# Optimization experiments

Measured on AMD Instinct MI355X. Metric: run time of the kernel, lower is better.

The kernel has to match this reference:

```python
import jax, jax.numpy as jnp
import numpy as np

WS = 16        # window size
NH = 8         # num heads
EPS = 1e-6
BN_EPS = 1e-5


def _l2norm(t):
    # normalize along the channel (d) axis, which is axis=-2, per position
    return t / jnp.linalg.norm(t, axis=-2, keepdims=True)


def setup_inputs() -> dict:
    key = jax.random.key(0)
    k1, k2, k3 = jax.random.split(key, 3)
    B, C, H, W = 8, 96, 256, 256
    x = jax.random.normal(k1, (B, C, H, W), dtype=jnp.float32)
    w_qkv = jax.random.normal(k2, (3 * C, C), dtype=jnp.float32) * (1.0 / np.sqrt(C))
    w_proj = jax.random.normal(k3, (C, C), dtype=jnp.float32) * (1.0 / np.sqrt(C))
    gamma = jnp.ones((C,), dtype=jnp.float32)
    beta = jnp.zeros((C,), dtype=jnp.float32)
    return {"x": x, "w_qkv": w_qkv, "w_proj": w_proj, "gamma": gamma, "beta": beta}


def reference(x, w_qkv, w_proj, gamma, beta):
    B, C, H, W = x.shape
    ws, nh = WS, NH
    d = C // nh
    # pad H, W up to multiples of ws (static shapes -> jit-safe)
    Hp = (H + ws - 1) // ws * ws
    Wp = (W + ws - 1) // ws * ws
    if (Hp, Wp) != (H, W):
        x = jnp.pad(x, ((0, 0), (0, 0), (0, Hp - H), (0, Wp - W)))
    hh, ww = Hp // ws, Wp // ws

    # 1x1 conv qkv projection (no bias)
    qkv = jnp.einsum('oc,bchw->bohw', w_qkv, x)  # [B, 3C, Hp, Wp]
    # rearrange 'b (qkv h d) (hh ws1) (ww ws2) -> qkv (b hh ww) h d (ws1 ws2)'
    qkv = qkv.reshape(B, 3, nh, d, hh, ws, ww, ws)
    qkv = qkv.transpose(1, 0, 4, 6, 2, 3, 5, 7).reshape(3, B * hh * ww, nh, d, ws * ws)
    q, k, v = qkv[0], qkv[1], qkv[2]  # each [bw, h, d, n]  (n = ws*ws)

    q = _l2norm(q).transpose(0, 1, 3, 2)  # [bw, h, n, d]
    k = _l2norm(k)                        # [bw, h, d, n]

    ksum = k.sum(axis=-1) + EPS           # [bw, h, d]
    tailor = 1.0 / (ws * ws + jnp.einsum('bhnc,bhc->bhn', q, ksum))  # [bw, h, n]

    kv = jnp.einsum('bhmn,bhcn->bhmc', k, v)     # [bw, h, d, d]
    attn = jnp.einsum('bhnm,bhmc->bhcn', q, kv)  # [bw, h, d, n]
    attn = attn + v.sum(axis=-1, keepdims=True)  # broadcast sum_n v over n
    attn = attn * tailor[:, :, None, :]

    # rearrange '(b hh ww) h d (ws1 ws2) -> b (h d) (hh ws1) (ww ws2)'
    out = attn.reshape(B, hh, ww, nh, d, ws, ws)
    out = out.transpose(0, 3, 4, 1, 5, 2, 6).reshape(B, C, Hp, Wp)
    out = out[:, :, :H, :W]

    # proj: 1x1 conv + BatchNorm2d (training-mode batch statistics)
    y = jnp.einsum('oc,bchw->bohw', w_proj, out)
    mean = y.mean(axis=(0, 2, 3), keepdims=True)
    var = y.var(axis=(0, 2, 3), keepdims=True)
    y = (y - mean) * jax.lax.rsqrt(var + BN_EPS)
    y = y * gamma[None, :, None, None] + beta[None, :, None, None]
    return y
```

## Files before the change

kernel.cpp:

```cpp
#include <hip/hip_runtime.h>

typedef short s8v __attribute__((ext_vector_type(8)));
typedef float f4v __attribute__((ext_vector_type(4)));

union F8 { int4 i; s8v s; };
union F8L { long long l[2]; s8v s; };

__device__ __forceinline__ short f2bf(float f){
  union {float f; unsigned u;} v; v.f = f;
  unsigned r = (v.u + 0x7FFFu + ((v.u >> 16) & 1u)) >> 16;
  return (short)r;
}

#define MFMA(a,b,c) __builtin_amdgcn_mfma_f32_16x16x32_bf16((a),(b),(c),0,0,0)

#define WS_W2_OFF   58368
#define WS_ST_OFF   82944
#define WS_OUT_OFF  (1u<<20)

__global__ void prep_kernel(const float* __restrict__ wqkv, const float* __restrict__ wproj,
                            unsigned short* __restrict__ w1, unsigned short* __restrict__ w2p,
                            float* __restrict__ stats){
  int i = blockIdx.x * 256 + threadIdx.x;
  for (int j = i; j < 304*96; j += gridDim.x * 256){
    int row = j / 96, c = j - row * 96;
    float v = (row < 288) ? wqkv[row * 96 + c] : 0.f;
    w1[j] = (unsigned short)f2bf(v);
  }
  for (int j = i; j < 96*128; j += gridDim.x * 256){
    int o = j >> 7, c = j & 127, h = c >> 4, ii = c & 15;
    float v = (ii < 12) ? wproj[o * 96 + h * 12 + ii] : 0.f;
    w2p[j] = (unsigned short)f2bf(v);
  }
  if (i < 192) stats[i] = 0.f;
}

__global__ __launch_bounds__(256,4) void attn_kernel(const float* __restrict__ x,
                                                     const unsigned short* __restrict__ w1,
                                                     short* __restrict__ outp){
  __shared__ short ks[2][16*264];
  __shared__ short vs[2][16*264];

  const int tid  = threadIdx.x;
  const int lane = tid & 63, wave = tid >> 6;
  const int quad = lane >> 4, col = lane & 15;
  const int wx = blockIdx.x, wy = blockIdx.y, b = blockIdx.z;
  const int h0 = wy * 16, w0 = wx * 16;

  for (int i = tid; i < 2*4*264; i += 256){
    int buf = i / (4*264), j = i % (4*264);
    int r = 12 + j / 264, cc = j % 264;
    short v = (r == 15) ? (short)0x3F80 : (short)0;
    ks[buf][r*264 + cc] = v; vs[buf][r*264 + cc] = v;
  }

  const float* xb = x + ((size_t)b * 96 << 16);
  s8v Bf[4][3];
  #pragma unroll
  for (int jt = 0; jt < 4; ++jt){
    int t0 = wave * 64 + jt * 16;
    const float* px = xb + (size_t)(h0 + (t0 >> 4)) * 256 + (w0 + col);
    #pragma unroll
    for (int kt = 0; kt < 3; ++kt){
      F8 f;
      #pragma unroll
      for (int j = 0; j < 8; ++j){
        int c = kt * 32 + quad * 8 + j;
        f.s[j] = f2bf(px[(size_t)c << 16]);
      }
      Bf[jt][kt] = f.s;
    }
  }

  for (int h = 0; h < 8; ++h){
    const int p = h & 1;
    s8v bq[4];
    {
      s8v Aq[3];
      #pragma unroll
      for (int kt = 0; kt < 3; ++kt){
        F8 f; f.i = *(const int4*)(w1 + (h*12 + col) * 96 + kt*32 + quad*8);
        Aq[kt] = f.s;
      }
      #pragma unroll
      for (int jt = 0; jt < 4; ++jt){
        f4v a = {0.f,0.f,0.f,0.f};
        #pragma unroll
        for (int kt = 0; kt < 3; ++kt) a = MFMA(Aq[kt], Bf[jt][kt], a);
        float s = (quad < 3) ? (a[0]*a[0] + a[1]*a[1] + a[2]*a[2] + a[3]*a[3]) : 0.f;
        s += __shfl_xor(s, 16, 64); s += __shfl_xor(s, 32, 64);
        float rq = rsqrtf(s);
        float q0 = a[0]*rq, q1 = a[1]*rq, q2 = a[2]*rq, q3 = a[3]*rq;
        int s0 = (quad == 0) ? col        : (32 + col);
        int s1 = (quad == 0) ? (16 + col) : (32 + col);
        float v0 = __shfl(q0, s0, 64), v1 = __shfl(q1, s0, 64);
        float v2 = __shfl(q2, s0, 64), v3 = __shfl(q3, s0, 64);
        float w4 = __shfl(q0, s1, 64), w5 = __shfl(q1, s1, 64);
        float w6 = __shfl(q2, s1, 64), w7 = __shfl(q3, s1, 64);
        F8 f;
        bool lo = (quad < 2);
        f.s[0] = lo ? f2bf(v0) : (short)0;
        f.s[1] = lo ? f2bf(v1) : (short)0;
        f.s[2] = lo ? f2bf(v2) : (short)0;
        f.s[3] = lo ? f2bf(v3) : (short)0;
        f.s[4] = (quad == 0) ? f2bf(w4) : ((quad == 1) ? (short)0x3F80 : (short)0);
        f.s[5] = (quad == 0) ? f2bf(w5) : (short)0;
        f.s[6] = (quad == 0) ? f2bf(w6) : (short)0;
        f.s[7] = (quad == 0) ? f2bf(w7) : (short)0;
        bq[jt] = f.s;
      }
    }
    {
      s8v Ak[3];
      #pragma unroll
      for (int kt = 0; kt < 3; ++kt){
        F8 f; f.i = *(const int4*)(w1 + (96 + h*12 + col) * 96 + kt*32 + quad*8);
        Ak[kt] = f.s;
      }
      #pragma unroll
      for (int jt = 0; jt < 4; ++jt){
        f4v a = {0.f,0.f,0.f,0.f};
        #pragma unroll
        for (int kt = 0; kt < 3; ++kt) a = MFMA(Ak[kt], Bf[jt][kt], a);
        float s = (quad < 3) ? (a[0]*a[0] + a[1]*a[1] + a[2]*a[2] + a[3]*a[3]) : 0.f;
        s += __shfl_xor(s, 16, 64); s += __shfl_xor(s, 32, 64);
        float rk = rsqrtf(s);
        if (quad < 3){
          int t = wave*64 + jt*16 + col;
          #pragma unroll
          for (int r = 0; r < 4; ++r) ks[p][(quad*4 + r)*264 + t] = f2bf(a[r]*rk);
        }
      }
    }
    {
      s8v Av[3];
      #pragma unroll
      for (int kt = 0; kt < 3; ++kt){
        F8 f; f.i = *(const int4*)(w1 + (192 + h*12 + col) * 96 + kt*32 + quad*8);
        Av[kt] = f.s;
      }
      #pragma unroll
      for (int jt = 0; jt < 4; ++jt){
        f4v a = {0.f,0.f,0.f,0.f};
        #pragma unroll
        for (int kt = 0; kt < 3; ++kt) a = MFMA(Av[kt], Bf[jt][kt], a);
        if (quad < 3){
          int t = wave*64 + jt*16 + col;
          #pragma unroll
          for (int r = 0; r < 4; ++r) vs[p][(quad*4 + r)*264 + t] = f2bf(a[r]);
        }
      }
    }
    __syncthreads();

    f4v kvv = {0.f,0.f,0.f,0.f};
    #pragma unroll
    for (int kk = 0; kk < 8; ++kk){
      F8 a, bv;
      a.i  = *(const int4*)&ks[p][col*264 + kk*32 + quad*8];
      bv.i = *(const int4*)&vs[p][col*264 + kk*32 + quad*8];
      kvv = MFMA(a.s, bv.s, kvv);
    }
    F8 fa;
    {
      int cc = (col == 12) ? 15 : col;
      int l0 = ((quad << 1) << 4) | cc;
      int l1 = (((quad << 1) + 1) << 4) | cc;
      float v;
      v = __shfl(kvv[0], l0 & 63, 64); fa.s[0] = f2bf((quad < 2) ? v : 0.f);
      v = __shfl(kvv[1], l0 & 63, 64); fa.s[1] = f2bf((quad < 2) ? v : 0.f);
      v = __shfl(kvv[2], l0 & 63, 64); fa.s[2] = f2bf((quad < 2) ? v : 0.f);
      v = __shfl(kvv[3], l0 & 63, 64); fa.s[3] = f2bf((quad < 2) ? v : 0.f);
      float v0  = __shfl(kvv[0], l1 & 63, 64);
      float v15 = __shfl(kvv[3], 48 | cc, 64);
      fa.s[4] = f2bf((quad == 0) ? v0 : ((quad == 1) ? v15 : 0.f));
      v = __shfl(kvv[1], l1 & 63, 64); fa.s[5] = f2bf((quad == 0) ? v : 0.f);
      v = __shfl(kvv[2], l1 & 63, 64); fa.s[6] = f2bf((quad == 0) ? v : 0.f);
      v = __shfl(kvv[3], l1 & 63, 64); fa.s[7] = f2bf((quad == 0) ? v : 0.f);
    }
    #pragma unroll
    for (int jt = 0; jt < 4; ++jt){
      int t0 = wave*64 + jt*16;
      f4v z = {0.f,0.f,0.f,0.f};
      f4v d2 = MFMA(fa.s, bq[jt], z);
      float dot = __shfl(d2[0], 48 + col, 64);
      float tl = 1.f / dot;
      if (quad < 3){
        int pix = (h0 + (t0 >> 4)) * 256 + (w0 + col);
        short* po = outp + ((size_t)((b*8 + h) * 65536 + pix)) * 12 + quad*4;
        short4 pk; pk.x = f2bf(d2[0]*tl); pk.y = f2bf(d2[1]*tl); pk.z = f2bf(d2[2]*tl); pk.w = f2bf(d2[3]*tl);
        *(short4*)po = pk;
      }
    }
  }
}

__device__ __forceinline__ void load_proj_bfrag(const short* __restrict__ outp,
                                                int b, int pixrow, int wave, int quad, int col,
                                                s8v Bf[4][4]){
  #pragma unroll
  for (int jt = 0; jt < 4; ++jt){
    int pix = pixrow + wave*64 + jt*16 + col;
    #pragma unroll
    for (int kt = 0; kt < 4; ++kt){
      int h = kt*2 + (quad >> 1);
      const short* pb = outp + ((size_t)((b*8 + h) * 65536 + pix)) * 12;
      F8L f;
      if ((quad & 1) == 0){ f.l[0] = *(const long long*)(pb);     f.l[1] = *(const long long*)(pb + 4); }
      else                { f.l[0] = *(const long long*)(pb + 8); f.l[1] = 0; }
      Bf[jt][kt] = f.s;
    }
  }
}

__global__ __launch_bounds__(256,4) void projstats_kernel(const short* __restrict__ outp,
                                                          const unsigned short* __restrict__ w2p,
                                                          float* __restrict__ stats){
  __shared__ float sld[192];
  const int tid = threadIdx.x;
  if (tid < 192) sld[tid] = 0.f;
  __syncthreads();
  const int lane = tid & 63, wave = tid >> 6;
  const int quad = lane >> 4, col = lane & 15;
  const int hrow = blockIdx.x, b = blockIdx.y;

  s8v Bf[4][4];
  load_proj_bfrag(outp, b, hrow*256, wave, quad, col, Bf);

  #pragma unroll
  for (int mt = 0; mt < 6; ++mt){
    s8v Af[4];
    #pragma unroll
    for (int kt = 0; kt < 4; ++kt){
      F8 f; f.i = *(const int4*)(w2p + (mt*16 + col)*128 + kt*32 + quad*8);
      Af[kt] = f.s;
    }
    float rs[4] = {0.f,0.f,0.f,0.f}, rss[4] = {0.f,0.f,0.f,0.f};
    #pragma unroll
    for (int jt = 0; jt < 4; ++jt){
      f4v a = {0.f,0.f,0.f,0.f};
      #pragma unroll
      for (int kt = 0; kt < 4; ++kt) a = MFMA(Af[kt], Bf[jt][kt], a);
      #pragma unroll
      for (int r = 0; r < 4; ++r){ float v = a[r]; rs[r] += v; rss[r] += v*v; }
    }
    #pragma unroll
    for (int r = 0; r < 4; ++r){
      float a1 = rs[r], a2 = rss[r];
      a1 += __shfl_xor(a1, 1, 64); a2 += __shfl_xor(a2, 1, 64);
      a1 += __shfl_xor(a1, 2, 64); a2 += __shfl_xor(a2, 2, 64);
      a1 += __shfl_xor(a1, 4, 64); a2 += __shfl_xor(a2, 4, 64);
      a1 += __shfl_xor(a1, 8, 64); a2 += __shfl_xor(a2, 8, 64);
      if (col == 0){
        int o = mt*16 + quad*4 + r;
        atomicAdd(&sld[o], a1);
        atomicAdd(&sld[96 + o], a2);
      }
    }
  }
  __syncthreads();
  if (tid < 192) atomicAdd(&stats[tid], sld[tid]);
}

__global__ __launch_bounds__(256,4) void projbn_kernel(const short* __restrict__ outp,
                                                       const unsigned short* __restrict__ w2p,
                                                       const float* __restrict__ stats,
                                                       const float* __restrict__ gamma,
                                                       const float* __restrict__ beta,
                                                       float* __restrict__ y){
  __shared__ float sc[96], sh[96];
  const int tid = threadIdx.x;
  if (tid < 96){
    const float invN = 1.f / 524288.f;
    float m  = stats[tid] * invN;
    float var = stats[96 + tid] * invN - m*m;
    float s = gamma[tid] * rsqrtf(var + 1e-5f);
    sc[tid] = s; sh[tid] = beta[tid] - m * s;
  }
  __syncthreads();
  const int lane = tid & 63, wave = tid >> 6;
  const int quad = lane >> 4, col = lane & 15;
  const int hrow = blockIdx.x, b = blockIdx.y;

  s8v Bf[4][4];
  load_proj_bfrag(outp, b, hrow*256, wave, quad, col, Bf);

  float* yb = y + ((size_t)(b*96) << 16) + (size_t)hrow * 256;
  #pragma unroll
  for (int mt = 0; mt < 6; ++mt){
    s8v Af[4];
    #pragma unroll
    for (int kt = 0; kt < 4; ++kt){
      F8 f; f.i = *(const int4*)(w2p + (mt*16 + col)*128 + kt*32 + quad*8);
      Af[kt] = f.s;
    }
    #pragma unroll
    for (int jt = 0; jt < 4; ++jt){
      int n0 = wave*64 + jt*16;
      f4v a = {0.f,0.f,0.f,0.f};
      #pragma unroll
      for (int kt = 0; kt < 4; ++kt) a = MFMA(Af[kt], Bf[jt][kt], a);
      #pragma unroll
      for (int r = 0; r < 4; ++r){
        int ch = mt*16 + quad*4 + r;
        yb[((size_t)ch << 16) + n0 + col] = a[r] * sc[ch] + sh[ch];
      }
    }
  }
}

extern "C" void kernel_launch(void* const* d_in, const int* in_sizes, int n_in,
                              void* d_out, int out_size, void* d_ws, size_t ws_size,
                              hipStream_t stream){
  const float* x     = (const float*)d_in[0];
  const float* wqkv  = (const float*)d_in[1];
  const float* wproj = (const float*)d_in[2];
  const float* gamma = (const float*)d_in[3];
  const float* beta  = (const float*)d_in[4];
  char* ws = (char*)d_ws;
  unsigned short* w1  = (unsigned short*)(ws);
  unsigned short* w2p = (unsigned short*)(ws + WS_W2_OFF);
  float* stats = (float*)(ws + WS_ST_OFF);
  short* outp  = (short*)(ws + WS_OUT_OFF);
  float* y = (float*)d_out;

  hipLaunchKernelGGL(prep_kernel, dim3(64), dim3(256), 0, stream, wqkv, wproj, w1, w2p, stats);
  hipLaunchKernelGGL(attn_kernel, dim3(16, 16, 8), dim3(256), 0, stream, x, w1, outp);
  hipLaunchKernelGGL(projstats_kernel, dim3(256, 8), dim3(256), 0, stream, outp, w2p, stats);
  hipLaunchKernelGGL(projbn_kernel, dim3(256, 8), dim3(256), 0, stream, outp, w2p, stats, gamma, beta, y);
}
```

Baseline: 543.3 us.

## Single-buffer attention LDS, halve proj tiles per block, and slice BN stat atomics

The attention kernel drops its K/V LDS double buffer in favour of one buffer plus an extra barrier per head, and its launch bounds are raised to 8 blocks per CU to allow higher occupancy. The projection kernels now give each block half a row of pixels (32 per wave), doubling the grid and halving register fragments, with launch bounds raised to 6. BatchNorm statistics are spread over 16 slices to reduce global atomic contention, and the BN kernel sums the slices. In exchange the attention kernel pays an extra barrier per head and loses overlap between heads.

```diff
diff --git a/kernel.cpp b/kernel.cpp
--- a/kernel.cpp
+++ b/kernel.cpp
@@ -16,6 +16,7 @@
 
 #define WS_W2_OFF   58368
 #define WS_ST_OFF   82944
+#define N_STAT_SLICES 16
 #define WS_OUT_OFF  (1u<<20)
 
 __global__ void prep_kernel(const float* __restrict__ wqkv, const float* __restrict__ wproj,
@@ -32,14 +33,14 @@
     float v = (ii < 12) ? wproj[o * 96 + h * 12 + ii] : 0.f;
     w2p[j] = (unsigned short)f2bf(v);
   }
-  if (i < 192) stats[i] = 0.f;
-}
-
-__global__ __launch_bounds__(256,4) void attn_kernel(const float* __restrict__ x,
+  if (i < 192 * N_STAT_SLICES) stats[i] = 0.f;
+}
+
+__global__ __launch_bounds__(256,8) void attn_kernel(const float* __restrict__ x,
                                                      const unsigned short* __restrict__ w1,
                                                      short* __restrict__ outp){
-  __shared__ short ks[2][16*264];
-  __shared__ short vs[2][16*264];
+  __shared__ short ks[16*264];
+  __shared__ short vs[16*264];
 
   const int tid  = threadIdx.x;
   const int lane = tid & 63, wave = tid >> 6;
@@ -47,11 +48,10 @@
   const int wx = blockIdx.x, wy = blockIdx.y, b = blockIdx.z;
   const int h0 = wy * 16, w0 = wx * 16;
 
-  for (int i = tid; i < 2*4*264; i += 256){
-    int buf = i / (4*264), j = i % (4*264);
-    int r = 12 + j / 264, cc = j % 264;
+  for (int i = tid; i < 4*264; i += 256){
+    int r = 12 + i / 264, cc = i % 264;
     short v = (r == 15) ? (short)0x3F80 : (short)0;
-    ks[buf][r*264 + cc] = v; vs[buf][r*264 + cc] = v;
+    ks[r*264 + cc] = v; vs[r*264 + cc] = v;
   }
 
   const float* xb = x + ((size_t)b * 96 << 16);
@@ -73,7 +73,6 @@
   }
 
   for (int h = 0; h < 8; ++h){
-    const int p = h & 1;
     s8v bq[4];
     {
       s8v Aq[3];
@@ -110,6 +109,7 @@
         bq[jt] = f.s;
       }
     }
+    __syncthreads();
     {
       s8v Ak[3];
       #pragma unroll
@@ -128,7 +128,7 @@
         if (quad < 3){
           int t = wave*64 + jt*16 + col;
           #pragma unroll
-          for (int r = 0; r < 4; ++r) ks[p][(quad*4 + r)*264 + t] = f2bf(a[r]*rk);
+          for (int r = 0; r < 4; ++r) ks[(quad*4 + r)*264 + t] = f2bf(a[r]*rk);
         }
       }
     }
@@ -147,7 +147,7 @@
         if (quad < 3){
           int t = wave*64 + jt*16 + col;
           #pragma unroll
-          for (int r = 0; r < 4; ++r) vs[p][(quad*4 + r)*264 + t] = f2bf(a[r]);
+          for (int r = 0; r < 4; ++r) vs[(quad*4 + r)*264 + t] = f2bf(a[r]);
         }
       }
     }
@@ -157,8 +157,8 @@
     #pragma unroll
     for (int kk = 0; kk < 8; ++kk){
       F8 a, bv;
-      a.i  = *(const int4*)&ks[p][col*264 + kk*32 + quad*8];
-      bv.i = *(const int4*)&vs[p][col*264 + kk*32 + quad*8];
+      a.i  = *(const int4*)&ks[col*264 + kk*32 + quad*8];
+      bv.i = *(const int4*)&vs[col*264 + kk*32 + quad*8];
       kvv = MFMA(a.s, bv.s, kvv);
     }
     F8 fa;
@@ -196,11 +196,11 @@
 }
 
 __device__ __forceinline__ void load_proj_bfrag(const short* __restrict__ outp,
-                                                int b, int pixrow, int wave, int quad, int col,
-                                                s8v Bf[4][4]){
+                                                int b, int pix0, int quad, int col,
+                                                s8v Bf[2][4]){
   #pragma unroll
-  for (int jt = 0; jt < 4; ++jt){
-    int pix = pixrow + wave*64 + jt*16 + col;
+  for (int jt = 0; jt < 2; ++jt){
+    int pix = pix0 + jt*16 + col;
     #pragma unroll
     for (int kt = 0; kt < 4; ++kt){
       int h = kt*2 + (quad >> 1);
@@ -213,7 +213,7 @@
   }
 }
 
-__global__ __launch_bounds__(256,4) void projstats_kernel(const short* __restrict__ outp,
+__global__ __launch_bounds__(256,6) void projstats_kernel(const short* __restrict__ outp,
                                                           const unsigned short* __restrict__ w2p,
                                                           float* __restrict__ stats){
   __shared__ float sld[192];
@@ -224,8 +224,8 @@
   const int quad = lane >> 4, col = lane & 15;
   const int hrow = blockIdx.x, b = blockIdx.y;
 
-  s8v Bf[4][4];
-  load_proj_bfrag(outp, b, hrow*256, wave, quad, col, Bf);
+  s8v Bf[2][4];
+  load_proj_bfrag(outp, b, hrow*128 + wave*32, quad, col, Bf);
 
   #pragma unroll
   for (int mt = 0; mt < 6; ++mt){
@@ -237,7 +237,7 @@
     }
     float rs[4] = {0.f,0.f,0.f,0.f}, rss[4] = {0.f,0.f,0.f,0.f};
     #pragma unroll
-    for (int jt = 0; jt < 4; ++jt){
+    for (int jt = 0; jt < 2; ++jt){
       f4v a = {0.f,0.f,0.f,0.f};
       #pragma unroll
       for (int kt = 0; kt < 4; ++kt) a = MFMA(Af[kt], Bf[jt][kt], a);
@@ -259,10 +259,10 @@
     }
   }
   __syncthreads();
-  if (tid < 192) atomicAdd(&stats[tid], sld[tid]);
-}
-
-__global__ __launch_bounds__(256,4) void projbn_kernel(const short* __restrict__ outp,
+  if (tid < 192) atomicAdd(&stats[(blockIdx.x & (N_STAT_SLICES-1))*192 + tid], sld[tid]);
+}
+
+__global__ __launch_bounds__(256,6) void projbn_kernel(const short* __restrict__ outp,
                                                        const unsigned short* __restrict__ w2p,
                                                        const float* __restrict__ stats,
                                                        const float* __restrict__ gamma,
@@ -271,9 +271,12 @@
   __shared__ float sc[96], sh[96];
   const int tid = threadIdx.x;
   if (tid < 96){
+    float s1 = 0.f, s2 = 0.f;
+    #pragma unroll
+    for (int s = 0; s < N_STAT_SLICES; ++s){ s1 += stats[s*192 + tid]; s2 += stats[s*192 + 96 + tid]; }
     const float invN = 1.f / 524288.f;
-    float m  = stats[tid] * invN;
-    float var = stats[96 + tid] * invN - m*m;
+    float m  = s1 * invN;
+    float var = s2 * invN - m*m;
     float s = gamma[tid] * rsqrtf(var + 1e-5f);
     sc[tid] = s; sh[tid] = beta[tid] - m * s;
   }
@@ -282,10 +285,10 @@
   const int quad = lane >> 4, col = lane & 15;
   const int hrow = blockIdx.x, b = blockIdx.y;
 
-  s8v Bf[4][4];
-  load_proj_bfrag(outp, b, hrow*256, wave, quad, col, Bf);
-
-  float* yb = y + ((size_t)(b*96) << 16) + (size_t)hrow * 256;
+  s8v Bf[2][4];
+  load_proj_bfrag(outp, b, hrow*128 + wave*32, quad, col, Bf);
+
+  float* yb = y + ((size_t)(b*96) << 16) + (size_t)hrow * 128;
   #pragma unroll
   for (int mt = 0; mt < 6; ++mt){
     s8v Af[4];
@@ -295,8 +298,8 @@
       Af[kt] = f.s;
     }
     #pragma unroll
-    for (int jt = 0; jt < 4; ++jt){
-      int n0 = wave*64 + jt*16;
+    for (int jt = 0; jt < 2; ++jt){
+      int n0 = wave*32 + jt*16;
       f4v a = {0.f,0.f,0.f,0.f};
       #pragma unroll
       for (int kt = 0; kt < 4; ++kt) a = MFMA(Af[kt], Bf[jt][kt], a);
@@ -326,6 +329,6 @@
 
   hipLaunchKernelGGL(prep_kernel, dim3(64), dim3(256), 0, stream, wqkv, wproj, w1, w2p, stats);
   hipLaunchKernelGGL(attn_kernel, dim3(16, 16, 8), dim3(256), 0, stream, x, w1, outp);
-  hipLaunchKernelGGL(projstats_kernel, dim3(256, 8), dim3(256), 0, stream, outp, w2p, stats);
-  hipLaunchKernelGGL(projbn_kernel, dim3(256, 8), dim3(256), 0, stream, outp, w2p, stats, gamma, beta, y);
-}
+  hipLaunchKernelGGL(projstats_kernel, dim3(512, 8), dim3(256), 0, stream, outp, w2p, stats);
+  hipLaunchKernelGGL(projbn_kernel, dim3(512, 8), dim3(256), 0, stream, outp, w2p, stats, gamma, beta, y);
+}
```

New measurement: 878.3 us. 61.7% more time.

## Store raw projection output as bf16 and apply BatchNorm in a streaming pass

Applied to the files above, without the earlier changes.

The projection kernel now also writes its pre-norm output as bf16 into a workspace buffer, so the final pass only streams that buffer and applies the scale and shift instead of reloading the attention output and redoing the projection matmul. Per-channel statistic atomics are spread over 16 slices to reduce contention on the global stats counters. The path runs only when the workspace holds the extra 96 MB buffer; otherwise it falls back to the old projbn kernel. It adds a bf16 rounding of the pre-norm values and extra write traffic in the stats pass.

```diff
diff --git a/kernel.cpp b/kernel.cpp
--- a/kernel.cpp
+++ b/kernel.cpp
@@ -12,11 +12,20 @@
   return (short)r;
 }
 
+__device__ __forceinline__ float bf2f(short s){
+  union {float f; unsigned u;} v; v.u = ((unsigned)(unsigned short)s) << 16;
+  return v.f;
+}
+
 #define MFMA(a,b,c) __builtin_amdgcn_mfma_f32_16x16x32_bf16((a),(b),(c),0,0,0)
 
 #define WS_W2_OFF   58368
 #define WS_ST_OFF   82944
+#define N_STAT_SLICES 16
 #define WS_OUT_OFF  (1u<<20)
+#define OUTP_BYTES  100663296u
+#define WS_YRAW_OFF (WS_OUT_OFF + OUTP_BYTES)
+#define WS_NEED_FUSED ((size_t)WS_YRAW_OFF + OUTP_BYTES)
 
 __global__ void prep_kernel(const float* __restrict__ wqkv, const float* __restrict__ wproj,
                             unsigned short* __restrict__ w1, unsigned short* __restrict__ w2p,
@@ -32,7 +41,7 @@
     float v = (ii < 12) ? wproj[o * 96 + h * 12 + ii] : 0.f;
     w2p[j] = (unsigned short)f2bf(v);
   }
-  if (i < 192) stats[i] = 0.f;
+  if (i < 192 * N_STAT_SLICES) stats[i] = 0.f;
 }
 
 __global__ __launch_bounds__(256,4) void attn_kernel(const float* __restrict__ x,
@@ -213,9 +222,10 @@
   }
 }
 
-__global__ __launch_bounds__(256,4) void projstats_kernel(const short* __restrict__ outp,
-                                                          const unsigned short* __restrict__ w2p,
-                                                          float* __restrict__ stats){
+__global__ __launch_bounds__(256,4) void projy_kernel(const short* __restrict__ outp,
+                                                      const unsigned short* __restrict__ w2p,
+                                                      float* __restrict__ stats,
+                                                      short* __restrict__ yraw){
   __shared__ float sld[192];
   const int tid = threadIdx.x;
   if (tid < 192) sld[tid] = 0.f;
@@ -227,6 +237,8 @@
   s8v Bf[4][4];
   load_proj_bfrag(outp, b, hrow*256, wave, quad, col, Bf);
 
+  short* yb = yraw ? (yraw + ((size_t)(b*96) << 16) + (size_t)hrow * 256) : (short*)0;
+
   #pragma unroll
   for (int mt = 0; mt < 6; ++mt){
     s8v Af[4];
@@ -243,6 +255,14 @@
       for (int kt = 0; kt < 4; ++kt) a = MFMA(Af[kt], Bf[jt][kt], a);
       #pragma unroll
       for (int r = 0; r < 4; ++r){ float v = a[r]; rs[r] += v; rss[r] += v*v; }
+      if (yb){
+        int n0 = wave*64 + jt*16;
+        #pragma unroll
+        for (int r = 0; r < 4; ++r){
+          int ch = mt*16 + quad*4 + r;
+          yb[((size_t)ch << 16) + n0 + col] = f2bf(a[r]);
+        }
+      }
     }
     #pragma unroll
     for (int r = 0; r < 4; ++r){
@@ -259,7 +279,49 @@
     }
   }
   __syncthreads();
-  if (tid < 192) atomicAdd(&stats[tid], sld[tid]);
+  if (tid < 192) atomicAdd(&stats[(blockIdx.x & (N_STAT_SLICES-1))*192 + tid], sld[tid]);
+}
+
+__device__ __forceinline__ void load_bn_coefs(const float* __restrict__ stats,
+                                              const float* __restrict__ gamma,
+                                              const float* __restrict__ beta,
+                                              float* sc, float* sh, int tid){
+  if (tid < 96){
+    float s1 = 0.f, s2 = 0.f;
+    #pragma unroll
+    for (int s = 0; s < N_STAT_SLICES; ++s){ s1 += stats[s*192 + tid]; s2 += stats[s*192 + 96 + tid]; }
+    const float invN = 1.f / 524288.f;
+    float m  = s1 * invN;
+    float var = s2 * invN - m*m;
+    float s = gamma[tid] * rsqrtf(var + 1e-5f);
+    sc[tid] = s; sh[tid] = beta[tid] - m * s;
+  }
+  __syncthreads();
+}
+
+__global__ __launch_bounds__(256,8) void bnapply_kernel(const short* __restrict__ yraw,
+                                                        const float* __restrict__ stats,
+                                                        const float* __restrict__ gamma,
+                                                        const float* __restrict__ beta,
+                                                        float* __restrict__ y){
+  __shared__ float sc[96], sh[96];
+  const int tid = threadIdx.x;
+  load_bn_coefs(stats, gamma, beta, sc, sh, tid);
+
+  const long long ngroups = (8LL*96*65536) / 8;
+  for (long long g = (long long)blockIdx.x * 256 + tid; g < ngroups; g += (long long)gridDim.x * 256){
+    long long base = g * 8;
+    int ch = (int)((base >> 16) % 96);
+    s8v v = *(const s8v*)(yraw + base);
+    float scc = sc[ch], shh = sh[ch];
+    f4v o0, o1;
+    #pragma unroll
+    for (int j = 0; j < 4; ++j) o0[j] = bf2f(v[j]) * scc + shh;
+    #pragma unroll
+    for (int j = 0; j < 4; ++j) o1[j] = bf2f(v[4+j]) * scc + shh;
+    *(f4v*)(y + base) = o0;
+    *(f4v*)(y + base + 4) = o1;
+  }
 }
 
 __global__ __launch_bounds__(256,4) void projbn_kernel(const short* __restrict__ outp,
@@ -270,14 +332,7 @@
                                                        float* __restrict__ y){
   __shared__ float sc[96], sh[96];
   const int tid = threadIdx.x;
-  if (tid < 96){
-    const float invN = 1.f / 524288.f;
-    float m  = stats[tid] * invN;
-    float var = stats[96 + tid] * invN - m*m;
-    float s = gamma[tid] * rsqrtf(var + 1e-5f);
-    sc[tid] = s; sh[tid] = beta[tid] - m * s;
-  }
-  __syncthreads();
+  load_bn_coefs(stats, gamma, beta, sc, sh, tid);
   const int lane = tid & 63, wave = tid >> 6;
   const int quad = lane >> 4, col = lane & 15;
   const int hrow = blockIdx.x, b = blockIdx.y;
@@ -324,8 +379,15 @@
   short* outp  = (short*)(ws + WS_OUT_OFF);
   float* y = (float*)d_out;
 
+  const bool fused = (ws_size >= WS_NEED_FUSED);
+  short* yraw = fused ? (short*)(ws + WS_YRAW_OFF) : (short*)0;
+
   hipLaunchKernelGGL(prep_kernel, dim3(64), dim3(256), 0, stream, wqkv, wproj, w1, w2p, stats);
   hipLaunchKernelGGL(attn_kernel, dim3(16, 16, 8), dim3(256), 0, stream, x, w1, outp);
-  hipLaunchKernelGGL(projstats_kernel, dim3(256, 8), dim3(256), 0, stream, outp, w2p, stats);
-  hipLaunchKernelGGL(projbn_kernel, dim3(256, 8), dim3(256), 0, stream, outp, w2p, stats, gamma, beta, y);
-}
+  hipLaunchKernelGGL(projy_kernel, dim3(256, 8), dim3(256), 0, stream, outp, w2p, stats, yraw);
+  if (fused){
+    hipLaunchKernelGGL(bnapply_kernel, dim3(2048), dim3(256), 0, stream, yraw, stats, gamma, beta, y);
+  } else {
+    hipLaunchKernelGGL(projbn_kernel, dim3(256, 8), dim3(256), 0, stream, outp, w2p, stats, gamma, beta, y);
+  }
+}
```

Result: no change. 552.1 us (+1.6%).
